# Performance work log

Measured on AMD Instinct MI355X. Metric: run time of the kernel, lower is better.

## Reference

```python
import jax, jax.numpy as jnp
import numpy as np


def setup_inputs() -> dict:
    key = jax.random.key(0)
    k1, k2 = jax.random.split(key)
    d, T, n = 256, 8192, 64
    # scale down so exp(ht^T D^T D hj) stays in range, as typical trained D would
    H = jax.random.normal(k1, (d, T), dtype=jnp.float32) * 0.1
    D = jax.random.normal(k2, (n, d), dtype=jnp.float32) * 0.1
    l2 = jnp.ones((), dtype=jnp.float32)
    return {"H": H, "D": D, "l2": l2}


def reference(H, D, l2):
    # H: [d, T], D: [n, d]
    DH = D @ H                                   # [n, T] = D @ H_T.T
    # S[t, j] = h_t^T (D^T D) h_j  == (DH)^T (DH)
    S = jnp.einsum('nt,nj->tj', DH, DH)          # [T, T]
    # beta_j = exp(-0.5 * ||D h_j||^2); row t: attn[t,:] = beta * exp(S[t,:]) / sum
    log_beta = -0.5 * jnp.sum(DH * DH, axis=0)   # [T]
    attn_map = jax.nn.softmax(S + log_beta[None, :], axis=1)  # [T, T]
    Z = l2 * (H @ attn_map)                      # [d, T]
    return Z
```

## Files before the change

### kernel.cpp

```cpp
#include <hip/hip_runtime.h>

#define T_DIM 8192
#define D_DIM 256
#define N_DIM 64
#define LOG2E 1.44269504f

typedef __bf16 bf16x8 __attribute__((ext_vector_type(8)));
typedef __bf16 bf16x4 __attribute__((ext_vector_type(4)));
typedef float f32x16 __attribute__((ext_vector_type(16)));

__device__ __forceinline__ f32x16 zero16() {
  f32x16 v;
#pragma unroll
  for (int i = 0; i < 16; ++i) v[i] = 0.f;
  return v;
}


__global__ __launch_bounds__(256) void k_dh(const float* __restrict__ H,
                                            const float* __restrict__ Dm,
                                            __bf16* __restrict__ DHf,
                                            float* __restrict__ lbe,
                                            float* __restrict__ rowsum) {
  __shared__ __bf16 HlThi[64 * 264];
  __shared__ __bf16 HlTlo[64 * 264];
  __shared__ __bf16 DHs[64 * 72];
  const int tid = threadIdx.x;
  const int t0 = blockIdx.x * 64;
  const int lane = tid & 63;
  const int wave = tid >> 6;
  const int h = lane >> 5;
  const int l31 = lane & 31;
  const float4* H4 = (const float4*)H;
#pragma unroll
  for (int r = 0; r < 16; ++r) {
    int idx = r * 256 + tid;
    int d = idx >> 4, tc = idx & 15;
    float4 v = H4[(size_t)d * (T_DIM / 4) + (t0 >> 2) + tc];
    float vv[4] = {v.x, v.y, v.z, v.w};
#pragma unroll
    for (int i = 0; i < 4; ++i) {
      __bf16 hi = (__bf16)vv[i];
      float lo = vv[i] - (float)hi;
      HlThi[(tc * 4 + i) * 264 + d] = hi;
      HlTlo[(tc * 4 + i) * 264 + d] = (__bf16)lo;
    }
  }
  __syncthreads();
  const int tt = wave & 1, nh = wave >> 1;
  const int m = tt * 32 + l31;
  const int n = nh * 32 + l31;
  f32x16 c = zero16();
  for (int kk = 0; kk < 16; ++kk) {
    bf16x8 ahi = *(const bf16x8*)&HlThi[m * 264 + kk * 16 + h * 8];
    bf16x8 alo = *(const bf16x8*)&HlTlo[m * 264 + kk * 16 + h * 8];
    const float4* dp = (const float4*)(Dm + (size_t)n * 256 + kk * 16 + h * 8);
    float4 b0 = dp[0], b1 = dp[1];
    float bv[8] = {b0.x, b0.y, b0.z, b0.w, b1.x, b1.y, b1.z, b1.w};
    bf16x8 bhi, blo;
#pragma unroll
    for (int i = 0; i < 8; ++i) {
      __bf16 hi = (__bf16)bv[i];
      bhi[i] = hi;
      blo[i] = (__bf16)(bv[i] - (float)hi);
    }
    c = __builtin_amdgcn_mfma_f32_32x32x16_bf16(ahi, bhi, c, 0, 0, 0);
    c = __builtin_amdgcn_mfma_f32_32x32x16_bf16(ahi, blo, c, 0, 0, 0);
    c = __builtin_amdgcn_mfma_f32_32x32x16_bf16(alo, bhi, c, 0, 0, 0);
  }
#pragma unroll
  for (int r = 0; r < 16; ++r) {
    int row = tt * 32 + (r & 3) + 8 * (r >> 2) + 4 * h;
    DHs[row * 72 + n] = (__bf16)c[r];
  }
  __syncthreads();
#pragma unroll
  for (int r = 0; r < 2; ++r) {
    int idx = r * 256 + tid;
    int g = idx >> 8, cc = (idx >> 5) & 7, l = idx & 31;
    bf16x8 w = *(const bf16x8*)&DHs[(g * 32 + l) * 72 + cc * 8];
    *(bf16x8*)(DHf + (size_t)(blockIdx.x * 2 + g) * 2048 + cc * 256 + l * 8) = w;
  }
  if (tid < 64) {
    float s = 0.f;
#pragma unroll
    for (int q = 0; q < 8; ++q) {
      bf16x8 w = *(const bf16x8*)&DHs[tid * 72 + q * 8];
#pragma unroll
      for (int i = 0; i < 8; ++i) { float f = (float)w[i]; s += f * f; }
    }
    lbe[t0 + tid] = -0.5f * s * LOG2E;
    rowsum[t0 + tid] = 0.f;
  }
}

__global__ __launch_bounds__(256, 2) void k_rowsum(const __bf16* __restrict__ DHf,
                                                   const float* __restrict__ lbe,
                                                   float* __restrict__ rowsum) {
  __shared__ float red2[64 * 65];
  const int tid = threadIdx.x;
  const int lane = tid & 63;
  const int wave = tid >> 6;
  const int h = lane >> 5;
  const int tt = wave & 1, jt = wave >> 1;
  const int t0 = (int)(blockIdx.x >> 4) * 64;
  const int jbase = (int)(blockIdx.x & 15) * 512;
  const int Gt = (t0 >> 5) + tt;
  bf16x8 aR[4];
#pragma unroll
  for (int kk = 0; kk < 4; ++kk)
    aR[kk] = *(const bf16x8*)(DHf + (size_t)Gt * 2048 + kk * 512 + lane * 8);
  float racc[16];
#pragma unroll
  for (int r = 0; r < 16; ++r) racc[r] = 0.f;
  for (int jit = 0; jit < 8; ++jit) {
    const size_t Gj = (jbase >> 5) + jit * 2 + jt;
    bf16x8 b[4];
#pragma unroll
    for (int kk = 0; kk < 4; ++kk)
      b[kk] = *(const bf16x8*)(DHf + Gj * 2048 + kk * 512 + lane * 8);
    const float lbv = lbe[jbase + jit * 64 + jt * 32 + (lane & 31)];
    f32x16 s = zero16();
#pragma unroll
    for (int kk = 0; kk < 4; ++kk)
      s = __builtin_amdgcn_mfma_f32_32x32x16_bf16(aR[kk], b[kk], s, 0, 0, 0);
#pragma unroll
    for (int r = 0; r < 16; ++r)
      racc[r] += __builtin_amdgcn_exp2f(__builtin_fmaf(s[r], LOG2E, lbv));
  }
#pragma unroll
  for (int r = 0; r < 16; ++r) {
    int tl = tt * 32 + (r & 3) + 8 * (r >> 2) + 4 * h;
    red2[tl * 65 + jt * 32 + (lane & 31)] = racc[r];
  }
  __syncthreads();
  if (tid < 64) {
    float s = 0.f;
#pragma unroll 8
    for (int c = 0; c < 64; ++c) s += red2[tid * 65 + c];
    atomicAdd(&rowsum[t0 + tid], s);
  }
}

__global__ __launch_bounds__(256) void k_scaleH(const float* __restrict__ H,
                                                const float* __restrict__ rowsum,
                                                __bf16* __restrict__ Hbf_sw,
                                                float* __restrict__ Z) {
  __shared__ float rinvL[64];
  const int tid = threadIdx.x;
  const int bx = blockIdx.x;
  const int tblk = bx >> 1, dh = bx & 1;
  const int t0 = tblk * 64;
  if (tid < 64) rinvL[tid] = 1.0f / rowsum[t0 + tid];
  __syncthreads();
#pragma unroll
  for (int itr = 0; itr < 4; ++itr) {
    int idx = itr * 256 + tid;
    int dl = idx >> 3, tbp = idx & 7;
    int d = dh * 128 + dl;
    int swz = (d ^ (d >> 3)) & 7;
    int tloc = (tbp ^ swz) << 3;
    const float4* hp = (const float4*)(H + (size_t)d * T_DIM + t0 + tloc);
    float4 v0 = hp[0], v1 = hp[1];
    float4 r0 = *(const float4*)&rinvL[tloc];
    float4 r1 = *(const float4*)&rinvL[tloc + 4];
    bf16x8 w;
    w[0] = (__bf16)(v0.x * r0.x); w[1] = (__bf16)(v0.y * r0.y);
    w[2] = (__bf16)(v0.z * r0.z); w[3] = (__bf16)(v0.w * r0.w);
    w[4] = (__bf16)(v1.x * r1.x); w[5] = (__bf16)(v1.y * r1.y);
    w[6] = (__bf16)(v1.z * r1.z); w[7] = (__bf16)(v1.w * r1.w);
    *(bf16x8*)(Hbf_sw + (size_t)tblk * 16384 + (size_t)d * 64 + tbp * 8) = w;
  }
  float4* Z4 = (float4*)Z;
  const int base = bx * 256 + tid;
  const float4 z4 = {0.f, 0.f, 0.f, 0.f};
#pragma unroll
  for (int r = 0; r < 8; ++r) Z4[r * 65536 + base] = z4;
}

__global__ __launch_bounds__(256, 2) void k_z(const __bf16* __restrict__ Hbf_sw,
                                              const __bf16* __restrict__ DHf,
                                              const float* __restrict__ lbe,
                                              const float* __restrict__ l2p,
                                              float* __restrict__ Z) {
  __shared__ __bf16 Hs[2][128 * 64];
  __shared__ __bf16 Pt[2][128 * 64];
  const int tid = threadIdx.x;
  const int lane = tid & 63;
  const int wave = tid >> 6;
  const int h = lane >> 5;
  const int l31 = lane & 31;
  const int bx = blockIdx.x;
  const int ts = bx & 3;
  const int dh = (bx >> 2) & 1;
  const int j0 = (bx >> 3) * 128;
  const float l2v = l2p[0];
  const int s_tt = wave & 1, s_jg = wave >> 1;
  bf16x8 bS[2][4];
  float lbv[2];
#pragma unroll
  for (int q = 0; q < 2; ++q) {
    const size_t Gj = (j0 >> 5) + s_jg * 2 + q;
#pragma unroll
    for (int kk = 0; kk < 4; ++kk)
      bS[q][kk] = *(const bf16x8*)(DHf + Gj * 2048 + kk * 512 + lane * 8);
    lbv[q] = lbe[j0 + (s_jg * 2 + q) * 32 + l31];
  }
  f32x16 acc[2][2];
#pragma unroll
  for (int u = 0; u < 2; ++u)
#pragma unroll
    for (int v = 0; v < 2; ++v) acc[u][v] = zero16();

#define DMA_HS(buf_, it_)                                                       \
  {                                                                             \
    const __bf16* gsrc =                                                        \
        Hbf_sw + (size_t)(ts * 32 + (it_)) * 16384 + (size_t)dh * 8192;         \
    _Pragma("unroll") for (int r = 0; r < 4; ++r) {                             \
      int chunk = wave * 4 + r;                                                 \
      __builtin_amdgcn_global_load_lds(                                         \
          (const __attribute__((address_space(1))) unsigned int*)(gsrc +        \
              chunk * 512 + lane * 8),                                          \
          (__attribute__((address_space(3))) unsigned int*)(&Hs[buf_][0] +      \
              chunk * 512),                                                     \
          16, 0, 0);                                                            \
    }                                                                           \
  }

#define S_PHASE(p_)                                                             \
  {                                                                             \
    _Pragma("unroll") for (int q = 0; q < 2; ++q) {                             \
      f32x16 s = zero16();                                                      \
      _Pragma("unroll") for (int kk = 0; kk < 4; ++kk)                          \
          s = __builtin_amdgcn_mfma_f32_32x32x16_bf16(aR[kk], bS[q][kk], s, 0,  \
                                                      0, 0);                    \
      const int jl = (s_jg * 2 + q) * 32 + l31;                                 \
      const int sj = (jl ^ (jl >> 3)) & 7;                                      \
      _Pragma("unroll") for (int g = 0; g < 4; ++g) {                           \
        const int tl = s_tt * 32 + g * 8 + 4 * h;                               \
        bf16x4 pv;                                                              \
        pv[0] = (__bf16)__builtin_amdgcn_exp2f(                                 \
            __builtin_fmaf(s[g * 4 + 0], LOG2E, lbv[q]));                       \
        pv[1] = (__bf16)__builtin_amdgcn_exp2f(                                 \
            __builtin_fmaf(s[g * 4 + 1], LOG2E, lbv[q]));                       \
        pv[2] = (__bf16)__builtin_amdgcn_exp2f(                                 \
            __builtin_fmaf(s[g * 4 + 2], LOG2E, lbv[q]));                       \
        pv[3] = (__bf16)__builtin_amdgcn_exp2f(                                 \
            __builtin_fmaf(s[g * 4 + 3], LOG2E, lbv[q]));                       \
        const int cchunk = tl >> 3;                                             \
        *(bf16x4*)&Pt[p_][jl * 64 + ((cchunk ^ sj) << 3) + 4 * h] = pv;         \
      }                                                                         \
    }                                                                           \
  }

  bf16x8 aR[4];
#pragma unroll
  for (int kk = 0; kk < 4; ++kk)
    aR[kk] = *(const bf16x8*)(DHf + (size_t)(ts * 64 + s_tt) * 2048 + kk * 512 + lane * 8);
  DMA_HS(0, 0);
  S_PHASE(0);
#pragma unroll
  for (int kk = 0; kk < 4; ++kk)
    aR[kk] = *(const bf16x8*)(DHf + (size_t)(ts * 64 + 2 + s_tt) * 2048 + kk * 512 + lane * 8);
  __syncthreads();

  for (int it = 0; it < 32; ++it) {
    const int p = it & 1;
    if (it < 31) {
      DMA_HS(p ^ 1, it + 1);
      S_PHASE(p ^ 1);
    }
    if (it < 30) {
      const size_t Gt = ts * 64 + (it + 2) * 2 + s_tt;
#pragma unroll
      for (int kk = 0; kk < 4; ++kk)
        aR[kk] = *(const bf16x8*)(DHf + Gt * 2048 + kk * 512 + lane * 8);
    }
#pragma unroll
    for (int kk = 0; kk < 4; ++kk) {
      const int c = kk * 2 + h;
      bf16x8 af[2], bw[2];
#pragma unroll
      for (int u = 0; u < 2; ++u) {
        int dl = (wave & 1) * 64 + u * 32 + l31;
        af[u] = *(const bf16x8*)&Hs[p][dl * 64 + ((c ^ ((dl ^ (dl >> 3)) & 7)) << 3)];
      }
#pragma unroll
      for (int v = 0; v < 2; ++v) {
        int j = (wave >> 1) * 64 + v * 32 + l31;
        bw[v] = *(const bf16x8*)&Pt[p][j * 64 + ((c ^ ((j ^ (j >> 3)) & 7)) << 3)];
      }
#pragma unroll
      for (int u = 0; u < 2; ++u)
#pragma unroll
        for (int v = 0; v < 2; ++v)
          acc[u][v] = __builtin_amdgcn_mfma_f32_32x32x16_bf16(af[u], bw[v], acc[u][v], 0, 0, 0);
    }
    __syncthreads();
  }
#undef S_PHASE
#undef DMA_HS
#pragma unroll
  for (int u = 0; u < 2; ++u)
#pragma unroll
    for (int v = 0; v < 2; ++v)
#pragma unroll
      for (int r = 0; r < 16; ++r) {
        int d = dh * 128 + (wave & 1) * 64 + u * 32 + (r & 3) + 8 * (r >> 2) + 4 * h;
        int j = j0 + (wave >> 1) * 64 + v * 32 + l31;
        atomicAdd(&Z[(size_t)d * T_DIM + j], acc[u][v][r] * l2v);
      }
}

extern "C" void kernel_launch(void* const* d_in, const int* in_sizes, int n_in,
                              void* d_out, int out_size, void* d_ws,
                              size_t ws_size, hipStream_t stream) {
  (void)in_sizes; (void)n_in; (void)out_size; (void)ws_size;
  const float* H = (const float*)d_in[0];
  const float* Dm = (const float*)d_in[1];
  const float* l2 = (const float*)d_in[2];
  float* Z = (float*)d_out;
  char* ws = (char*)d_ws;
  __bf16* DHf = (__bf16*)ws;
  float* lbe = (float*)(ws + 1048576);
  float* rowsum = (float*)(ws + 1048576 + 32768);
  __bf16* Hbf_sw = (__bf16*)(ws + 1048576 + 65536);

  k_dh<<<128, 256, 0, stream>>>(H, Dm, DHf, lbe, rowsum);
  k_rowsum<<<2048, 256, 0, stream>>>(DHf, lbe, rowsum);
  k_scaleH<<<256, 256, 0, stream>>>(H, rowsum, Hbf_sw, Z);
  k_z<<<512, 256, 0, stream>>>(Hbf_sw, DHf, lbe, l2, Z);
}
```

Baseline: 161.5 us.

## Restructure attention-output kernel: full-d tiles, 512 threads, partial-sum reduction

The Z kernel now has each 512-thread block cover all 256 d rows for a 128-wide j tile. This halves the split across d and removes the duplicated S/exp recomputation that the two d-halves used to do. H is stored in a chunked [c][d][8] layout so LDS reads need no swizzle. When the workspace is large enough, the Z atomics are replaced by per-split partial buffers plus a separate reduction kernel, and the rowsum kernel gains register prefetch of the next B tile, split MFMA accumulators and higher occupancy. The partial path writes and then reads 64MB of extra traffic, and the unswizzled LDS layout may bring bank conflicts.

New measurement: 290.1 us. +79.6%, slower.

```diff
diff --git a/kernel.cpp b/kernel.cpp
--- a/kernel.cpp
+++ b/kernel.cpp
@@ -94,7 +94,7 @@
   }
 }
 
-__global__ __launch_bounds__(256, 2) void k_rowsum(const __bf16* __restrict__ DHf,
+__global__ __launch_bounds__(256, 4) void k_rowsum(const __bf16* __restrict__ DHf,
                                                    const float* __restrict__ lbe,
                                                    float* __restrict__ rowsum) {
   __shared__ float red2[64 * 65];
@@ -113,20 +113,36 @@
   float racc[16];
 #pragma unroll
   for (int r = 0; r < 16; ++r) racc[r] = 0.f;
-  for (int jit = 0; jit < 8; ++jit) {
-    const size_t Gj = (jbase >> 5) + jit * 2 + jt;
-    bf16x8 b[4];
+  bf16x8 b[4];
+  {
+    const size_t Gj = (size_t)(jbase >> 5) + jt;
 #pragma unroll
     for (int kk = 0; kk < 4; ++kk)
       b[kk] = *(const bf16x8*)(DHf + Gj * 2048 + kk * 512 + lane * 8);
+  }
+#pragma unroll
+  for (int jit = 0; jit < 8; ++jit) {
+    bf16x8 bn[4];
+    if (jit < 7) {
+      const size_t Gj = (size_t)(jbase >> 5) + (jit + 1) * 2 + jt;
+#pragma unroll
+      for (int kk = 0; kk < 4; ++kk)
+        bn[kk] = *(const bf16x8*)(DHf + Gj * 2048 + kk * 512 + lane * 8);
+    }
     const float lbv = lbe[jbase + jit * 64 + jt * 32 + (lane & 31)];
-    f32x16 s = zero16();
-#pragma unroll
-    for (int kk = 0; kk < 4; ++kk)
-      s = __builtin_amdgcn_mfma_f32_32x32x16_bf16(aR[kk], b[kk], s, 0, 0, 0);
+    f32x16 s0 = zero16(), s1 = zero16();
+    s0 = __builtin_amdgcn_mfma_f32_32x32x16_bf16(aR[0], b[0], s0, 0, 0, 0);
+    s1 = __builtin_amdgcn_mfma_f32_32x32x16_bf16(aR[1], b[1], s1, 0, 0, 0);
+    s0 = __builtin_amdgcn_mfma_f32_32x32x16_bf16(aR[2], b[2], s0, 0, 0, 0);
+    s1 = __builtin_amdgcn_mfma_f32_32x32x16_bf16(aR[3], b[3], s1, 0, 0, 0);
 #pragma unroll
     for (int r = 0; r < 16; ++r)
-      racc[r] += __builtin_amdgcn_exp2f(__builtin_fmaf(s[r], LOG2E, lbv));
+      racc[r] += __builtin_amdgcn_exp2f(
+          __builtin_fmaf(s0[r] + s1[r], LOG2E, lbv));
+    if (jit < 7) {
+#pragma unroll
+      for (int kk = 0; kk < 4; ++kk) b[kk] = bn[kk];
+    }
   }
 #pragma unroll
   for (int r = 0; r < 16; ++r) {
@@ -144,68 +160,67 @@
 
 __global__ __launch_bounds__(256) void k_scaleH(const float* __restrict__ H,
                                                 const float* __restrict__ rowsum,
-                                                __bf16* __restrict__ Hbf_sw,
-                                                float* __restrict__ Z) {
-  __shared__ float rinvL[64];
+                                                __bf16* __restrict__ Hbf,
+                                                float* __restrict__ Z,
+                                                int zeroZ) {
+  __shared__ float rinvL[32];
   const int tid = threadIdx.x;
-  const int bx = blockIdx.x;
-  const int tblk = bx >> 1, dh = bx & 1;
-  const int t0 = tblk * 64;
-  if (tid < 64) rinvL[tid] = 1.0f / rowsum[t0 + tid];
-  __syncthreads();
-#pragma unroll
-  for (int itr = 0; itr < 4; ++itr) {
-    int idx = itr * 256 + tid;
-    int dl = idx >> 3, tbp = idx & 7;
-    int d = dh * 128 + dl;
-    int swz = (d ^ (d >> 3)) & 7;
-    int tloc = (tbp ^ swz) << 3;
-    const float4* hp = (const float4*)(H + (size_t)d * T_DIM + t0 + tloc);
-    float4 v0 = hp[0], v1 = hp[1];
-    float4 r0 = *(const float4*)&rinvL[tloc];
-    float4 r1 = *(const float4*)&rinvL[tloc + 4];
+  const int tblk = blockIdx.x;
+  const int t0 = tblk * 32;
+  if (tid < 32) rinvL[tid] = 1.0f / rowsum[t0 + tid];
+  __syncthreads();
+  const int d = tid;
+  const float4* hp = (const float4*)(H + (size_t)d * T_DIM + t0);
+#pragma unroll
+  for (int c = 0; c < 4; ++c) {
+    float4 v0 = hp[c * 2], v1 = hp[c * 2 + 1];
+    const float4 r0 = *(const float4*)&rinvL[c * 8];
+    const float4 r1 = *(const float4*)&rinvL[c * 8 + 4];
     bf16x8 w;
     w[0] = (__bf16)(v0.x * r0.x); w[1] = (__bf16)(v0.y * r0.y);
     w[2] = (__bf16)(v0.z * r0.z); w[3] = (__bf16)(v0.w * r0.w);
     w[4] = (__bf16)(v1.x * r1.x); w[5] = (__bf16)(v1.y * r1.y);
     w[6] = (__bf16)(v1.z * r1.z); w[7] = (__bf16)(v1.w * r1.w);
-    *(bf16x8*)(Hbf_sw + (size_t)tblk * 16384 + (size_t)d * 64 + tbp * 8) = w;
-  }
-  float4* Z4 = (float4*)Z;
-  const int base = bx * 256 + tid;
-  const float4 z4 = {0.f, 0.f, 0.f, 0.f};
-#pragma unroll
-  for (int r = 0; r < 8; ++r) Z4[r * 65536 + base] = z4;
-}
-
-__global__ __launch_bounds__(256, 2) void k_z(const __bf16* __restrict__ Hbf_sw,
+    *(bf16x8*)(Hbf + (size_t)tblk * 8192 + c * 2048 + d * 8) = w;
+  }
+  if (zeroZ) {
+    float4* Z4 = (float4*)Z;
+    const float4 z4 = {0.f, 0.f, 0.f, 0.f};
+    const int base = blockIdx.x * 256 + tid;
+#pragma unroll
+    for (int r = 0; r < 8; ++r) Z4[r * 65536 + base] = z4;
+  }
+}
+
+__global__ __launch_bounds__(512, 4) void k_z(const __bf16* __restrict__ Hbf,
                                               const __bf16* __restrict__ DHf,
                                               const float* __restrict__ lbe,
                                               const float* __restrict__ l2p,
-                                              float* __restrict__ Z) {
-  __shared__ __bf16 Hs[2][128 * 64];
-  __shared__ __bf16 Pt[2][128 * 64];
+                                              float* __restrict__ Z,
+                                              float* __restrict__ Zp,
+                                              int useAtomic) {
+  __shared__ __bf16 Hs[2][4][256][8];
+  __shared__ __bf16 Pt[2][4][128][8];
   const int tid = threadIdx.x;
   const int lane = tid & 63;
   const int wave = tid >> 6;
   const int h = lane >> 5;
   const int l31 = lane & 31;
   const int bx = blockIdx.x;
-  const int ts = bx & 3;
-  const int dh = (bx >> 2) & 1;
+  const int ts = bx & 7;
   const int j0 = (bx >> 3) * 128;
+  const int jh = wave & 3, kh = wave >> 2;
+  const int dq = wave & 3, jv = wave >> 2;
+  const int tb0 = ts * 32;
   const float l2v = l2p[0];
-  const int s_tt = wave & 1, s_jg = wave >> 1;
-  bf16x8 bS[2][4];
-  float lbv[2];
-#pragma unroll
-  for (int q = 0; q < 2; ++q) {
-    const size_t Gj = (j0 >> 5) + s_jg * 2 + q;
+  bf16x8 bS[4];
+  {
+    const size_t Gj = (size_t)(j0 >> 5) + jh;
 #pragma unroll
     for (int kk = 0; kk < 4; ++kk)
-      bS[q][kk] = *(const bf16x8*)(DHf + Gj * 2048 + kk * 512 + lane * 8);
-    lbv[q] = lbe[j0 + (s_jg * 2 + q) * 32 + l31];
-  }
+      bS[kk] = *(const bf16x8*)(DHf + Gj * 2048 + kk * 512 + lane * 8);
+  }
+  const float lbv = lbe[j0 + jh * 32 + l31];
   f32x16 acc[2][2];
 #pragma unroll
   for (int u = 0; u < 2; ++u)
@@ -214,54 +229,54 @@
 
 #define DMA_HS(buf_, it_)                                                       \
   {                                                                             \
-    const __bf16* gsrc =                                                        \
-        Hbf_sw + (size_t)(ts * 32 + (it_)) * 16384 + (size_t)dh * 8192;         \
-    _Pragma("unroll") for (int r = 0; r < 4; ++r) {                             \
-      int chunk = wave * 4 + r;                                                 \
+    const __bf16* gsrc = Hbf + (size_t)(tb0 + (it_)) * 8192;                    \
+    _Pragma("unroll") for (int r = 0; r < 2; ++r) {                             \
+      const int slot = r * 512 + tid;                                           \
       __builtin_amdgcn_global_load_lds(                                         \
           (const __attribute__((address_space(1))) unsigned int*)(gsrc +        \
-              chunk * 512 + lane * 8),                                          \
-          (__attribute__((address_space(3))) unsigned int*)(&Hs[buf_][0] +      \
-              chunk * 512),                                                     \
+              slot * 8),                                                        \
+          (__attribute__((address_space(3))) unsigned int*)(                    \
+              &Hs[buf_][0][0][0] + slot * 8),                                   \
           16, 0, 0);                                                            \
     }                                                                           \
   }
 
+#define LOAD_AR(it_)                                                            \
+  {                                                                             \
+    const size_t Gt_ = (size_t)(tb0 + (it_));                                   \
+    _Pragma("unroll") for (int kk = 0; kk < 4; ++kk)                            \
+        aR[kk] = *(const bf16x8*)(DHf + Gt_ * 2048 + kk * 512 + lane * 8);      \
+  }
+
 #define S_PHASE(p_)                                                             \
   {                                                                             \
-    _Pragma("unroll") for (int q = 0; q < 2; ++q) {                             \
-      f32x16 s = zero16();                                                      \
-      _Pragma("unroll") for (int kk = 0; kk < 4; ++kk)                          \
-          s = __builtin_amdgcn_mfma_f32_32x32x16_bf16(aR[kk], bS[q][kk], s, 0,  \
-                                                      0, 0);                    \
-      const int jl = (s_jg * 2 + q) * 32 + l31;                                 \
-      const int sj = (jl ^ (jl >> 3)) & 7;                                      \
-      _Pragma("unroll") for (int g = 0; g < 4; ++g) {                           \
-        const int tl = s_tt * 32 + g * 8 + 4 * h;                               \
-        bf16x4 pv;                                                              \
-        pv[0] = (__bf16)__builtin_amdgcn_exp2f(                                 \
-            __builtin_fmaf(s[g * 4 + 0], LOG2E, lbv[q]));                       \
-        pv[1] = (__bf16)__builtin_amdgcn_exp2f(                                 \
-            __builtin_fmaf(s[g * 4 + 1], LOG2E, lbv[q]));                       \
-        pv[2] = (__bf16)__builtin_amdgcn_exp2f(                                 \
-            __builtin_fmaf(s[g * 4 + 2], LOG2E, lbv[q]));                       \
-        pv[3] = (__bf16)__builtin_amdgcn_exp2f(                                 \
-            __builtin_fmaf(s[g * 4 + 3], LOG2E, lbv[q]));                       \
-        const int cchunk = tl >> 3;                                             \
-        *(bf16x4*)&Pt[p_][jl * 64 + ((cchunk ^ sj) << 3) + 4 * h] = pv;         \
-      }                                                                         \
+    f32x16 s0_ = zero16(), s1_ = zero16();                                      \
+    s0_ = __builtin_amdgcn_mfma_f32_32x32x16_bf16(aR[0], bS[0], s0_, 0, 0, 0);  \
+    s1_ = __builtin_amdgcn_mfma_f32_32x32x16_bf16(aR[1], bS[1], s1_, 0, 0, 0);  \
+    s0_ = __builtin_amdgcn_mfma_f32_32x32x16_bf16(aR[2], bS[2], s0_, 0, 0, 0);  \
+    s1_ = __builtin_amdgcn_mfma_f32_32x32x16_bf16(aR[3], bS[3], s1_, 0, 0, 0);  \
+    const int jl_ = jh * 32 + l31;                                              \
+    _Pragma("unroll") for (int g2 = 0; g2 < 2; ++g2) {                          \
+      const int g_ = kh * 2 + g2;                                               \
+      const int r_ = g_ * 4;                                                    \
+      bf16x4 pv_;                                                               \
+      pv_[0] = (__bf16)__builtin_amdgcn_exp2f(                                  \
+          __builtin_fmaf(s0_[r_ + 0] + s1_[r_ + 0], LOG2E, lbv));               \
+      pv_[1] = (__bf16)__builtin_amdgcn_exp2f(                                  \
+          __builtin_fmaf(s0_[r_ + 1] + s1_[r_ + 1], LOG2E, lbv));               \
+      pv_[2] = (__bf16)__builtin_amdgcn_exp2f(                                  \
+          __builtin_fmaf(s0_[r_ + 2] + s1_[r_ + 2], LOG2E, lbv));               \
+      pv_[3] = (__bf16)__builtin_amdgcn_exp2f(                                  \
+          __builtin_fmaf(s0_[r_ + 3] + s1_[r_ + 3], LOG2E, lbv));               \
+      *(bf16x4*)(&Pt[p_][g_][jl_][4 * h]) = pv_;                                \
     }                                                                           \
   }
 
   bf16x8 aR[4];
-#pragma unroll
-  for (int kk = 0; kk < 4; ++kk)
-    aR[kk] = *(const bf16x8*)(DHf + (size_t)(ts * 64 + s_tt) * 2048 + kk * 512 + lane * 8);
+  LOAD_AR(0);
   DMA_HS(0, 0);
   S_PHASE(0);
-#pragma unroll
-  for (int kk = 0; kk < 4; ++kk)
-    aR[kk] = *(const bf16x8*)(DHf + (size_t)(ts * 64 + 2 + s_tt) * 2048 + kk * 512 + lane * 8);
+  LOAD_AR(1);
   __syncthreads();
 
   for (int it = 0; it < 32; ++it) {
@@ -270,52 +285,75 @@
       DMA_HS(p ^ 1, it + 1);
       S_PHASE(p ^ 1);
     }
-    if (it < 30) {
-      const size_t Gt = ts * 64 + (it + 2) * 2 + s_tt;
-#pragma unroll
-      for (int kk = 0; kk < 4; ++kk)
-        aR[kk] = *(const bf16x8*)(DHf + Gt * 2048 + kk * 512 + lane * 8);
-    }
-#pragma unroll
-    for (int kk = 0; kk < 4; ++kk) {
+    if (it < 30) LOAD_AR(it + 2);
+#pragma unroll
+    for (int kk = 0; kk < 2; ++kk) {
       const int c = kk * 2 + h;
       bf16x8 af[2], bw[2];
 #pragma unroll
-      for (int u = 0; u < 2; ++u) {
-        int dl = (wave & 1) * 64 + u * 32 + l31;
-        af[u] = *(const bf16x8*)&Hs[p][dl * 64 + ((c ^ ((dl ^ (dl >> 3)) & 7)) << 3)];
-      }
-#pragma unroll
-      for (int v = 0; v < 2; ++v) {
-        int j = (wave >> 1) * 64 + v * 32 + l31;
-        bw[v] = *(const bf16x8*)&Pt[p][j * 64 + ((c ^ ((j ^ (j >> 3)) & 7)) << 3)];
-      }
-#pragma unroll
       for (int u = 0; u < 2; ++u)
+        af[u] = *(const bf16x8*)(&Hs[p][c][dq * 64 + u * 32 + l31][0]);
+#pragma unroll
+      for (int v = 0; v < 2; ++v)
+        bw[v] = *(const bf16x8*)(&Pt[p][c][jv * 64 + v * 32 + l31][0]);
+#pragma unroll
+      for (int u = 0; u < 2; ++u)
 #pragma unroll
         for (int v = 0; v < 2; ++v)
-          acc[u][v] = __builtin_amdgcn_mfma_f32_32x32x16_bf16(af[u], bw[v], acc[u][v], 0, 0, 0);
+          acc[u][v] = __builtin_amdgcn_mfma_f32_32x32x16_bf16(af[u], bw[v],
+                                                              acc[u][v], 0, 0, 0);
     }
     __syncthreads();
   }
 #undef S_PHASE
+#undef LOAD_AR
 #undef DMA_HS
-#pragma unroll
-  for (int u = 0; u < 2; ++u)
-#pragma unroll
-    for (int v = 0; v < 2; ++v)
-#pragma unroll
-      for (int r = 0; r < 16; ++r) {
-        int d = dh * 128 + (wave & 1) * 64 + u * 32 + (r & 3) + 8 * (r >> 2) + 4 * h;
-        int j = j0 + (wave >> 1) * 64 + v * 32 + l31;
-        atomicAdd(&Z[(size_t)d * T_DIM + j], acc[u][v][r] * l2v);
-      }
+  if (useAtomic) {
+#pragma unroll
+    for (int u = 0; u < 2; ++u)
+#pragma unroll
+      for (int v = 0; v < 2; ++v)
+#pragma unroll
+        for (int r = 0; r < 16; ++r) {
+          int d = dq * 64 + u * 32 + (r & 3) + 8 * (r >> 2) + 4 * h;
+          int j = j0 + jv * 64 + v * 32 + l31;
+          atomicAdd(&Z[(size_t)d * T_DIM + j], acc[u][v][r] * l2v);
+        }
+  } else {
+    float* zp = Zp + (size_t)ts * (256 * (size_t)T_DIM);
+#pragma unroll
+    for (int u = 0; u < 2; ++u)
+#pragma unroll
+      for (int v = 0; v < 2; ++v)
+#pragma unroll
+        for (int r = 0; r < 16; ++r) {
+          int d = dq * 64 + u * 32 + (r & 3) + 8 * (r >> 2) + 4 * h;
+          int j = j0 + jv * 64 + v * 32 + l31;
+          zp[(size_t)d * T_DIM + j] = acc[u][v][r];
+        }
+  }
+}
+
+__global__ __launch_bounds__(256) void k_zred(const float* __restrict__ Zp,
+                                              const float* __restrict__ l2p,
+                                              float* __restrict__ Z) {
+  const int i = blockIdx.x * 256 + threadIdx.x;
+  const float l2v = l2p[0];
+  const float4* zp4 = (const float4*)Zp;
+  float4 a = zp4[i];
+#pragma unroll
+  for (int s = 1; s < 8; ++s) {
+    float4 b = zp4[(size_t)s * 524288 + i];
+    a.x += b.x; a.y += b.y; a.z += b.z; a.w += b.w;
+  }
+  float4 o = {a.x * l2v, a.y * l2v, a.z * l2v, a.w * l2v};
+  ((float4*)Z)[i] = o;
 }
 
 extern "C" void kernel_launch(void* const* d_in, const int* in_sizes, int n_in,
                               void* d_out, int out_size, void* d_ws,
                               size_t ws_size, hipStream_t stream) {
-  (void)in_sizes; (void)n_in; (void)out_size; (void)ws_size;
+  (void)in_sizes; (void)n_in; (void)out_size;
   const float* H = (const float*)d_in[0];
   const float* Dm = (const float*)d_in[1];
   const float* l2 = (const float*)d_in[2];
@@ -324,10 +362,14 @@
   __bf16* DHf = (__bf16*)ws;
   float* lbe = (float*)(ws + 1048576);
   float* rowsum = (float*)(ws + 1048576 + 32768);
-  __bf16* Hbf_sw = (__bf16*)(ws + 1048576 + 65536);
+  __bf16* Hbf = (__bf16*)(ws + 1114112);
+  float* Zp = (float*)(ws + 5308416);
+  const size_t need = 5308416ull + 67108864ull;
+  const int usePartial = (ws_size >= need) ? 1 : 0;
 
   k_dh<<<128, 256, 0, stream>>>(H, Dm, DHf, lbe, rowsum);
   k_rowsum<<<2048, 256, 0, stream>>>(DHf, lbe, rowsum);
-  k_scaleH<<<256, 256, 0, stream>>>(H, rowsum, Hbf_sw, Z);
-  k_z<<<512, 256, 0, stream>>>(Hbf_sw, DHf, lbe, l2, Z);
-}
+  k_scaleH<<<256, 256, 0, stream>>>(H, rowsum, Hbf, Z, usePartial ? 0 : 1);
+  k_z<<<512, 512, 0, stream>>>(Hbf, DHf, lbe, l2, Z, Zp, usePartial ? 0 : 1);
+  if (usePartial) k_zred<<<2048, 256, 0, stream>>>(Zp, l2, Z);
+}
```

## Restructure rowsum kernel: 8 waves per block, each owning a t-tile with prefetched j-tiles

Applied to the files above, without the earlier changes.

The row-sum kernel now runs 512-thread blocks where each of 8 waves owns its own 32-row t-tile and walks all 16 j-tiles of the block's 512-column slice. Previously 4 waves split 2 t-tiles by 2 j-tiles. It also software-prefetches the next j-tile's B fragments into registers while the current tile's MFMAs and exps run. The aim is fewer blocks, fewer atomics per row and hidden global-load latency, at the cost of more registers for the double-buffered fragments and a larger shared reduction buffer.

New measurement: 159.7 us. No clear change (-1.1%).

```diff
diff --git a/kernel.cpp b/kernel.cpp
--- a/kernel.cpp
+++ b/kernel.cpp
@@ -94,50 +94,64 @@
   }
 }
 
-__global__ __launch_bounds__(256, 2) void k_rowsum(const __bf16* __restrict__ DHf,
+__global__ __launch_bounds__(512, 4) void k_rowsum(const __bf16* __restrict__ DHf,
                                                    const float* __restrict__ lbe,
                                                    float* __restrict__ rowsum) {
-  __shared__ float red2[64 * 65];
+  __shared__ float red2[256][33];
   const int tid = threadIdx.x;
   const int lane = tid & 63;
   const int wave = tid >> 6;
   const int h = lane >> 5;
-  const int tt = wave & 1, jt = wave >> 1;
-  const int t0 = (int)(blockIdx.x >> 4) * 64;
+  const int l31 = lane & 31;
+  const int t0 = (int)(blockIdx.x >> 4) * 256;
   const int jbase = (int)(blockIdx.x & 15) * 512;
-  const int Gt = (t0 >> 5) + tt;
+  const size_t Gt = (size_t)(t0 >> 5) + wave;
   bf16x8 aR[4];
 #pragma unroll
   for (int kk = 0; kk < 4; ++kk)
-    aR[kk] = *(const bf16x8*)(DHf + (size_t)Gt * 2048 + kk * 512 + lane * 8);
+    aR[kk] = *(const bf16x8*)(DHf + Gt * 2048 + kk * 512 + lane * 8);
   float racc[16];
 #pragma unroll
   for (int r = 0; r < 16; ++r) racc[r] = 0.f;
-  for (int jit = 0; jit < 8; ++jit) {
-    const size_t Gj = (jbase >> 5) + jit * 2 + jt;
-    bf16x8 b[4];
+  bf16x8 b[4];
+  {
+    const size_t Gj = (size_t)(jbase >> 5);
 #pragma unroll
     for (int kk = 0; kk < 4; ++kk)
       b[kk] = *(const bf16x8*)(DHf + Gj * 2048 + kk * 512 + lane * 8);
-    const float lbv = lbe[jbase + jit * 64 + jt * 32 + (lane & 31)];
+  }
+  for (int jit = 0; jit < 16; ++jit) {
+    bf16x8 bn[4];
+    if (jit < 15) {
+      const size_t Gj = (size_t)(jbase >> 5) + jit + 1;
+#pragma unroll
+      for (int kk = 0; kk < 4; ++kk)
+        bn[kk] = *(const bf16x8*)(DHf + Gj * 2048 + kk * 512 + lane * 8);
+    }
+    const float lbv = lbe[jbase + jit * 32 + l31];
     f32x16 s = zero16();
-#pragma unroll
-    for (int kk = 0; kk < 4; ++kk)
-      s = __builtin_amdgcn_mfma_f32_32x32x16_bf16(aR[kk], b[kk], s, 0, 0, 0);
+    s = __builtin_amdgcn_mfma_f32_32x32x16_bf16(aR[0], b[0], s, 0, 0, 0);
+    s = __builtin_amdgcn_mfma_f32_32x32x16_bf16(aR[1], b[1], s, 0, 0, 0);
+    s = __builtin_amdgcn_mfma_f32_32x32x16_bf16(aR[2], b[2], s, 0, 0, 0);
+    s = __builtin_amdgcn_mfma_f32_32x32x16_bf16(aR[3], b[3], s, 0, 0, 0);
 #pragma unroll
     for (int r = 0; r < 16; ++r)
       racc[r] += __builtin_amdgcn_exp2f(__builtin_fmaf(s[r], LOG2E, lbv));
+    if (jit < 15) {
+#pragma unroll
+      for (int kk = 0; kk < 4; ++kk) b[kk] = bn[kk];
+    }
   }
 #pragma unroll
   for (int r = 0; r < 16; ++r) {
-    int tl = tt * 32 + (r & 3) + 8 * (r >> 2) + 4 * h;
-    red2[tl * 65 + jt * 32 + (lane & 31)] = racc[r];
-  }
-  __syncthreads();
-  if (tid < 64) {
+    int tl = wave * 32 + (r & 3) + 8 * (r >> 2) + 4 * h;
+    red2[tl][l31] = racc[r];
+  }
+  __syncthreads();
+  if (tid < 256) {
     float s = 0.f;
 #pragma unroll 8
-    for (int c = 0; c < 64; ++c) s += red2[tid * 65 + c];
+    for (int c = 0; c < 32; ++c) s += red2[tid][c];
     atomicAdd(&rowsum[t0 + tid], s);
   }
 }
@@ -327,7 +341,7 @@
   __bf16* Hbf_sw = (__bf16*)(ws + 1048576 + 65536);
 
   k_dh<<<128, 256, 0, stream>>>(H, Dm, DHf, lbe, rowsum);
-  k_rowsum<<<2048, 256, 0, stream>>>(DHf, lbe, rowsum);
+  k_rowsum<<<512, 512, 0, stream>>>(DHf, lbe, rowsum);
   k_scaleH<<<256, 256, 0, stream>>>(H, rowsum, Hbf_sw, Z);
   k_z<<<512, 256, 0, stream>>>(Hbf_sw, DHf, lbe, l2, Z);
 }
```
